# Optimization experiments

Measured on AMD Instinct MI355X. Metric: run time of the kernel, lower is better.

## Reference

```python
import jax, jax.numpy as jnp
import numpy as np

N_NODES = 100000
N_EDGES = 3200000
N_GRAPHS = 512
DIM_H = 128
N_LAYERS = 3
N_CLASSES = 10
BN_EPS = 1e-5


def setup_inputs() -> dict:
    key = jax.random.key(0)
    ks = jax.random.split(key, 16)
    s = 1.0 / np.sqrt(DIM_H)
    x = jax.random.normal(ks[0], (N_NODES, DIM_H), dtype=jnp.float32)
    edge_index = jax.random.randint(ks[1], (2, N_EDGES), 0, N_NODES, dtype=jnp.int64)
    batch = jnp.sort(jax.random.randint(ks[2], (N_NODES,), 0, N_GRAPHS, dtype=jnp.int64))
    W1 = jax.random.uniform(ks[3], (N_LAYERS, DIM_H, DIM_H), jnp.float32, -s, s)
    b1 = jax.random.uniform(ks[4], (N_LAYERS, DIM_H), jnp.float32, -s, s)
    gamma = jnp.ones((N_LAYERS, DIM_H), jnp.float32)
    beta = jnp.zeros((N_LAYERS, DIM_H), jnp.float32)
    rmean = 0.1 * jax.random.normal(ks[5], (N_LAYERS, DIM_H), dtype=jnp.float32)
    rvar = jax.random.uniform(ks[6], (N_LAYERS, DIM_H), jnp.float32, 0.5, 1.5)
    W2 = jax.random.uniform(ks[7], (N_LAYERS, DIM_H, DIM_H), jnp.float32, -s, s)
    b2 = jax.random.uniform(ks[8], (N_LAYERS, DIM_H), jnp.float32, -s, s)
    dcat = DIM_H * N_LAYERS
    sf = 1.0 / np.sqrt(dcat)
    Wfin = jax.random.uniform(ks[9], (dcat, dcat), jnp.float32, -sf, sf)
    bfin = jax.random.uniform(ks[10], (dcat,), jnp.float32, -sf, sf)
    Wout = jax.random.uniform(ks[11], (dcat, N_CLASSES), jnp.float32, -sf, sf)
    bout = jax.random.uniform(ks[12], (N_CLASSES,), jnp.float32, -sf, sf)
    return {"x": x, "edge_index": edge_index, "batch": batch, "num_layers": N_LAYERS,
            "W1": W1, "b1": b1, "gamma": gamma, "beta": beta, "rmean": rmean, "rvar": rvar,
            "W2": W2, "b2": b2, "Wfin": Wfin, "bfin": bfin, "Wout": Wout, "bout": bout}


def reference(x, edge_index, batch, num_layers, W1, b1, gamma, beta, rmean, rvar, W2, b2, Wfin, bfin, Wout, bout):
    src, dst = edge_index[0], edge_index[1]
    h = x
    pooled = []
    for i in range(num_layers):
        # GINConv (eps=0): MLP(x + sum_{j in N(i)} x_j)
        aggr = jax.ops.segment_sum(h[src], dst, num_segments=N_NODES)
        z = (h + aggr) @ W1[i] + b1[i]
        # BatchNorm1d in eval mode (running stats)
        z = gamma[i] * (z - rmean[i]) * jax.lax.rsqrt(rvar[i] + BN_EPS) + beta[i]
        z = jax.nn.relu(z)
        h = jax.nn.relu(z @ W2[i] + b2[i])
        # global_add_pool: segment-sum over graph ids
        pooled.append(jax.ops.segment_sum(h, batch, num_segments=N_GRAPHS))
    h_fin = jnp.concatenate(pooled, axis=1)  # [G, dim_h*num_layers]
    h_fin = jax.nn.relu(h_fin @ Wfin + bfin)
    # dropout p=0.5 is identity in eval mode
    logits = h_fin @ Wout + bout
    return logits, jax.nn.log_softmax(logits, axis=1)
```

## Files before the change

### kernel.cpp

```cpp
#include <hip/hip_runtime.h>
#include <stdint.h>

#define N_NODES 100000
#define N_EDGES 3200000
#define N_GRAPHS 512
#define DIM 128
#define M_PAD 100096
#define NGB (M_PAD / 256)
#define NBUCK 391
#define CAP 9216
#define TILE 4096
#define NTILE 782
#define XMM_NB 392

typedef __bf16 bf16x8 __attribute__((ext_vector_type(8)));
typedef float f32x4 __attribute__((ext_vector_type(4)));

__device__ __forceinline__ unsigned short f2bf(float f) {
  unsigned u = __float_as_uint(f);
  u = u + 0x7FFFu + ((u >> 16) & 1u);
  return (unsigned short)(u >> 16);
}
__device__ __forceinline__ float bflo(unsigned v) { return __uint_as_float(v << 16); }
__device__ __forceinline__ float bfhi(unsigned v) { return __uint_as_float(v & 0xFFFF0000u); }
__device__ __forceinline__ unsigned packbf(float a, float b) {
  return (unsigned)f2bf(a) | ((unsigned)f2bf(b) << 16);
}

__global__ void k_zero32(int* __restrict__ p, int n) {
  int i = blockIdx.x * 256 + threadIdx.x;
  if (i < n) p[i] = 0;
}

__global__ __launch_bounds__(256) void k_bucket(const int* __restrict__ ei,
                                                int* __restrict__ cnt,
                                                unsigned* __restrict__ rec) {
  __shared__ int hist[NBUCK];
  __shared__ int curs[NBUCK];
  int t = threadIdx.x;
  int base_e = blockIdx.x * TILE;
  int es[16], ed[16];
#pragma unroll
  for (int k = 0; k < 16; ++k) {
    int e = base_e + k * 256 + t;
    if (e < N_EDGES) { es[k] = ei[e]; ed[k] = ei[N_EDGES + e]; }
    else ed[k] = -1;
  }
  for (int i = t; i < NBUCK; i += 256) hist[i] = 0;
  __syncthreads();
#pragma unroll
  for (int k = 0; k < 16; ++k)
    if (ed[k] >= 0) atomicAdd(&hist[ed[k] >> 8], 1);
  __syncthreads();
  for (int i = t; i < NBUCK; i += 256) {
    int h = hist[i];
    int g = h ? atomicAdd(&cnt[i], h) : 0;
    curs[i] = i * CAP + g;
  }
  __syncthreads();
#pragma unroll
  for (int k = 0; k < 16; ++k) {
    if (ed[k] >= 0) {
      int b = ed[k] >> 8;
      int pos = atomicAdd(&curs[b], 1);
      rec[pos] = ((unsigned)es[k] << 8) | (unsigned)(ed[k] & 255);
    }
  }
}

__global__ __launch_bounds__(512) void k_bscan(const int* __restrict__ cnt,
                                               int* __restrict__ bbase,
                                               int* __restrict__ row_ptr) {
  __shared__ int sc[512];
  int t = threadIdx.x;
  int tot = (t < NBUCK) ? min(cnt[t], CAP) : 0;
  sc[t] = tot; __syncthreads();
  for (int off = 1; off < 512; off <<= 1) {
    int x = (t >= off) ? sc[t - off] : 0;
    __syncthreads();
    sc[t] += x;
    __syncthreads();
  }
  if (t < NBUCK) bbase[t] = sc[t] - tot;
  if (t == NBUCK - 1) {
    bbase[NBUCK] = sc[t];
    row_ptr[N_NODES] = sc[t];
  }
}

__global__ __launch_bounds__(256) void k_build(const unsigned* __restrict__ rec,
                                               const int* __restrict__ cnt,
                                               const int* __restrict__ bbase,
                                               int* __restrict__ row_ptr,
                                               int* __restrict__ col) {
  __shared__ int hist[256];
  __shared__ int sc[256];
  __shared__ int curs[256];
  int b = blockIdx.x, t = threadIdx.x;
  int n = min(cnt[b], CAP);
  const unsigned* p = rec + (size_t)b * CAP;
  hist[t] = 0; __syncthreads();
  for (int i = t; i < n; i += 256) atomicAdd(&hist[p[i] & 255u], 1);
  __syncthreads();
  int v = hist[t];
  sc[t] = v; __syncthreads();
  for (int off = 1; off < 256; off <<= 1) {
    int x = (t >= off) ? sc[t - off] : 0;
    __syncthreads();
    sc[t] += x;
    __syncthreads();
  }
  int excl = bbase[b] + sc[t] - v;
  int node = (b << 8) + t;
  if (node < N_NODES) row_ptr[node] = excl;
  curs[t] = excl;
  __syncthreads();
  for (int i = t; i < n; i += 256) {
    unsigned w = p[i];
    int pos = atomicAdd(&curs[w & 255u], 1);
    col[pos] = (int)(w >> 8);
  }
}

__global__ void k_gptr(const int* __restrict__ batch, int* __restrict__ gptr) {
  int g = blockIdx.x * 64 + threadIdx.x;
  if (g > N_GRAPHS) return;
  int lo = 0, hi = N_NODES;
  while (lo < hi) { int mid = (lo + hi) >> 1; if (batch[mid] < g) lo = mid + 1; else hi = mid; }
  gptr[g] = lo;
}

__global__ __launch_bounds__(256) void k_xmm1(const float* __restrict__ x,
                                              float* __restrict__ pmax,
                                              float* __restrict__ pmin) {
  __shared__ float smx[8][32][4];
  __shared__ float smn[8][32][4];
  int t = threadIdx.x;
  int c4 = t & 31;
  int ro = t >> 5;
  float mx0 = 0.f, mx1 = 0.f, mx2 = 0.f, mx3 = 0.f;
  float mn0 = 0.f, mn1 = 0.f, mn2 = 0.f, mn3 = 0.f;
  for (int row = blockIdx.x * 8 + ro; row < N_NODES; row += XMM_NB * 8) {
    float4 v = ((const float4*)x)[(size_t)row * 32 + c4];
    mx0 = fmaxf(mx0, v.x); mn0 = fmaxf(mn0, -v.x);
    mx1 = fmaxf(mx1, v.y); mn1 = fmaxf(mn1, -v.y);
    mx2 = fmaxf(mx2, v.z); mn2 = fmaxf(mn2, -v.z);
    mx3 = fmaxf(mx3, v.w); mn3 = fmaxf(mn3, -v.w);
  }
  smx[ro][c4][0] = mx0; smx[ro][c4][1] = mx1; smx[ro][c4][2] = mx2; smx[ro][c4][3] = mx3;
  smn[ro][c4][0] = mn0; smn[ro][c4][1] = mn1; smn[ro][c4][2] = mn2; smn[ro][c4][3] = mn3;
  __syncthreads();
  for (int off = 4; off > 0; off >>= 1) {
    if (ro < off) {
#pragma unroll
      for (int k = 0; k < 4; ++k) {
        smx[ro][c4][k] = fmaxf(smx[ro][c4][k], smx[ro + off][c4][k]);
        smn[ro][c4][k] = fmaxf(smn[ro][c4][k], smn[ro + off][c4][k]);
      }
    }
    __syncthreads();
  }
  if (ro == 0) {
#pragma unroll
    for (int k = 0; k < 4; ++k) {
      pmax[blockIdx.x * 128 + c4 * 4 + k] = smx[0][c4][k];
      pmin[blockIdx.x * 128 + c4 * 4 + k] = smn[0][c4][k];
    }
  }
}

__global__ __launch_bounds__(64) void k_xmm2(const float* __restrict__ pmax,
                                             const float* __restrict__ pmin,
                                             float* __restrict__ xmx,
                                             float* __restrict__ xminf) {
  int c = blockIdx.x & 127;
  int isMin = blockIdx.x >> 7;
  const float* src = isMin ? pmin : pmax;
  int l = threadIdx.x;
  float m = 0.f;
  for (int p2 = l; p2 < XMM_NB; p2 += 64) m = fmaxf(m, src[p2 * 128 + c]);
#pragma unroll
  for (int off = 32; off > 0; off >>= 1) m = fmaxf(m, __shfl_down(m, off));
  if (l == 0) {
    if (isMin) xminf[c] = -m;
    else xmx[c] = m;
  }
}

__global__ __launch_bounds__(64) void k_hred(const float* __restrict__ pmaxb,
                                             float* __restrict__ hmax) {
  int c = blockIdx.x;
  float m = 0.f;
  for (int b = threadIdx.x; b < NGB; b += 64) m = fmaxf(m, pmaxb[(size_t)b * 128 + c]);
#pragma unroll
  for (int off = 32; off > 0; off >>= 1) m = fmaxf(m, __shfl_down(m, off));
  if (threadIdx.x == 0) hmax[c] = m;
}

__global__ void k_convx(const float* __restrict__ x, const float* __restrict__ qmin,
                        const float* __restrict__ qmax, unsigned short* __restrict__ xq) {
  int i = blockIdx.x * 256 + threadIdx.x;
  if (i >= M_PAD * 64) return;
  int lane = i & 63;
  unsigned short o = 0;
  if ((i >> 6) < N_NODES) {
    float mn0 = qmin[2 * lane], mn1 = qmin[2 * lane + 1];
    float r0 = qmax[2 * lane] - mn0, r1 = qmax[2 * lane + 1] - mn1;
    float is0 = r0 > 1e-20f ? 255.f / r0 : 0.f;
    float is1 = r1 > 1e-20f ? 255.f / r1 : 0.f;
    float2 f = ((const float2*)x)[i];
    int q0 = (int)rintf((f.x - mn0) * is0); q0 = min(max(q0, 0), 255);
    int q1 = (int)rintf((f.y - mn1) * is1); q1 = min(max(q1, 0), 255);
    o = (unsigned short)(q0 | (q1 << 8));
  }
  xq[i] = o;
}

__global__ void k_quant(const unsigned* __restrict__ hbf, const float* __restrict__ qmax,
                        unsigned short* __restrict__ hq) {
  int i = blockIdx.x * 256 + threadIdx.x;
  if (i >= M_PAD * 64) return;
  int lane = i & 63;
  float mx0 = qmax[2 * lane], mx1 = qmax[2 * lane + 1];
  float is0 = mx0 > 1e-20f ? 255.f / mx0 : 0.f;
  float is1 = mx1 > 1e-20f ? 255.f / mx1 : 0.f;
  unsigned v = hbf[i];
  int q0 = (int)rintf(bflo(v) * is0); q0 = min(max(q0, 0), 255);
  int q1 = (int)rintf(bfhi(v) * is1); q1 = min(max(q1, 0), 255);
  hq[i] = (unsigned short)(q0 | (q1 << 8));
}

__global__ void k_convw(const float* __restrict__ W1, const float* __restrict__ W2,
                        unsigned short* __restrict__ Wt1, unsigned short* __restrict__ Wt2) {
  int i = blockIdx.x * 256 + threadIdx.x;
  if (i >= 3 * DIM * DIM) return;
  int l = i >> 14, rem = i & 16383, k = rem >> 7, n = rem & 127;
  int o = (l << 14) + (n << 7) + k;
  Wt1[o] = f2bf(W1[i]);
  Wt2[o] = f2bf(W2[i]);
}

__global__ void k_coef(const float* __restrict__ b1, const float* __restrict__ gamma,
                       const float* __restrict__ beta, const float* __restrict__ rmean,
                       const float* __restrict__ rvar, const float* __restrict__ b2,
                       float* __restrict__ sA1, float* __restrict__ sB1,
                       float* __restrict__ sA2, float* __restrict__ sB2) {
  int i = blockIdx.x * 128 + threadIdx.x;
  if (i >= 3 * DIM) return;
  float sa = gamma[i] * rsqrtf(rvar[i] + 1e-5f);
  sA1[i] = sa;
  sB1[i] = fmaf(sa, b1[i] - rmean[i], beta[i]);
  sA2[i] = 1.0f;
  sB2[i] = b2[i];
}

__global__ __launch_bounds__(256) void k_aggr(const unsigned short* __restrict__ hq,
                                              const int* __restrict__ row_ptr,
                                              const int* __restrict__ col,
                                              const float* __restrict__ qmin,
                                              const float* __restrict__ qmax,
                                              unsigned* __restrict__ tmp) {
  int wv = (blockIdx.x << 2) + (threadIdx.x >> 6);
  int lane = threadIdx.x & 63;
  if (wv >= M_PAD) return;
  if (wv >= N_NODES) { tmp[wv * 64 + lane] = 0u; return; }
  float mn0 = qmin[2 * lane], mn1 = qmin[2 * lane + 1];
  float sc0 = (qmax[2 * lane] - mn0) * (1.0f / 255.0f);
  float sc1 = (qmax[2 * lane + 1] - mn1) * (1.0f / 255.0f);
  unsigned sv = hq[(size_t)wv * 64 + lane];
  int ia0 = (int)(sv & 255u), ia1 = (int)(sv >> 8);
  int s = __builtin_amdgcn_readfirstlane(row_ptr[wv]);
  int e = __builtin_amdgcn_readfirstlane(row_ptr[wv + 1]);
  for (int base = s; base < e; base += 64) {
    int n = e - base; if (n > 64) n = 64;
    int cv = (lane < n) ? col[base + lane] : 0;
    int j = 0;
    for (; j + 8 <= n; j += 8) {
      int c0 = __builtin_amdgcn_readlane(cv, j + 0);
      int c1 = __builtin_amdgcn_readlane(cv, j + 1);
      int c2 = __builtin_amdgcn_readlane(cv, j + 2);
      int c3 = __builtin_amdgcn_readlane(cv, j + 3);
      int c4 = __builtin_amdgcn_readlane(cv, j + 4);
      int c5 = __builtin_amdgcn_readlane(cv, j + 5);
      int c6 = __builtin_amdgcn_readlane(cv, j + 6);
      int c7 = __builtin_amdgcn_readlane(cv, j + 7);
      unsigned v0 = hq[(size_t)c0 * 64 + lane];
      unsigned v1 = hq[(size_t)c1 * 64 + lane];
      unsigned v2 = hq[(size_t)c2 * 64 + lane];
      unsigned v3 = hq[(size_t)c3 * 64 + lane];
      unsigned v4 = hq[(size_t)c4 * 64 + lane];
      unsigned v5 = hq[(size_t)c5 * 64 + lane];
      unsigned v6 = hq[(size_t)c6 * 64 + lane];
      unsigned v7 = hq[(size_t)c7 * 64 + lane];
      ia0 += (int)(v0 & 255u) + (int)(v1 & 255u) + (int)(v2 & 255u) + (int)(v3 & 255u)
           + (int)(v4 & 255u) + (int)(v5 & 255u) + (int)(v6 & 255u) + (int)(v7 & 255u);
      ia1 += (int)(v0 >> 8) + (int)(v1 >> 8) + (int)(v2 >> 8) + (int)(v3 >> 8)
           + (int)(v4 >> 8) + (int)(v5 >> 8) + (int)(v6 >> 8) + (int)(v7 >> 8);
    }
    for (; j < n; ++j) {
      int c = __builtin_amdgcn_readlane(cv, j);
      unsigned v = hq[(size_t)c * 64 + lane];
      ia0 += (int)(v & 255u); ia1 += (int)(v >> 8);
    }
  }
  float cnt = (float)(e - s + 1);
  float A0 = fmaf(mn0, cnt, sc0 * (float)ia0);
  float A1 = fmaf(mn1, cnt, sc1 * (float)ia1);
  tmp[wv * 64 + lane] = packbf(A0, A1);
}

__global__ __launch_bounds__(256, 2) void k_gemm(const unsigned short* __restrict__ A,
                                                 const unsigned short* __restrict__ Wt,
                                                 const float* __restrict__ sA,
                                                 const float* __restrict__ sB,
                                                 unsigned short* __restrict__ out,
                                                 float* __restrict__ pmaxb, int do_max) {
  __shared__ float colred[128];
  int w = threadIdx.x >> 6, lane = threadIdx.x & 63;
  int q = lane >> 4, n16 = lane & 15;
  int rbase = (blockIdx.x << 8) + (w << 6);
  if (do_max && threadIdx.x < 128) colred[threadIdx.x] = 0.f;

  bf16x8 Bf[4][8];
#pragma unroll
  for (int ks = 0; ks < 4; ++ks)
#pragma unroll
    for (int c = 0; c < 8; ++c)
      Bf[ks][c] = *(const bf16x8*)(Wt + (size_t)((c << 4) + n16) * DIM + ks * 32 + q * 8);

  float sc = sA[(0 << 4) + n16];
  (void)sc;
  float mcol[8];
#pragma unroll
  for (int c = 0; c < 8; ++c) mcol[c] = 0.f;

#pragma unroll
  for (int t = 0; t < 4; ++t) {
    int r0 = rbase + (t << 4);
    f32x4 acc[8] = {};
#pragma unroll
    for (int ks = 0; ks < 4; ++ks) {
      bf16x8 a = *(const bf16x8*)(A + (size_t)(r0 + n16) * DIM + ks * 32 + q * 8);
#pragma unroll
      for (int c = 0; c < 8; ++c)
        acc[c] = __builtin_amdgcn_mfma_f32_16x16x32_bf16(a, Bf[ks][c], acc[c], 0, 0, 0);
    }
#pragma unroll
    for (int c = 0; c < 8; ++c) {
      int colc = (c << 4) + n16;
      float s = sA[colc], tt = sB[colc];
#pragma unroll
      for (int r = 0; r < 4; ++r) {
        float v = fmaxf(fmaf(s, acc[c][r], tt), 0.0f);
        mcol[c] = fmaxf(mcol[c], v);
        out[(size_t)(r0 + (q << 2) + r) * DIM + colc] = f2bf(v);
      }
    }
  }

  if (do_max) {
    __syncthreads();
#pragma unroll
    for (int c = 0; c < 8; ++c)
      atomicMax((int*)&colred[(c << 4) + n16], __float_as_int(mcol[c]));
    __syncthreads();
    if (threadIdx.x < 128)
      pmaxb[(size_t)blockIdx.x * 128 + threadIdx.x] = colred[threadIdx.x];
  }
}

__global__ __launch_bounds__(256) void k_pool(const unsigned* __restrict__ hbf,
                                              const int* __restrict__ gptr,
                                              float* __restrict__ pooled, int layer) {
  __shared__ float red[4][128];
  int g = blockIdx.x;
  int uc = threadIdx.x & 63, rs = threadIdx.x >> 6;
  int beg = gptr[g], end = gptr[g + 1];
  float a0 = 0.f, a1 = 0.f;
  for (int r = beg + rs; r < end; r += 4) {
    unsigned v = hbf[(size_t)r * 64 + uc];
    a0 += bflo(v); a1 += bfhi(v);
  }
  red[rs][2 * uc] = a0; red[rs][2 * uc + 1] = a1;
  __syncthreads();
  if (rs == 0) {
    int c0 = 2 * uc, c1 = 2 * uc + 1;
    pooled[(size_t)g * 384 + layer * DIM + c0] = red[0][c0] + red[1][c0] + red[2][c0] + red[3][c0];
    pooled[(size_t)g * 384 + layer * DIM + c1] = red[0][c1] + red[1][c1] + red[2][c1] + red[3][c1];
  }
}

__global__ __launch_bounds__(384) void k_head(const float* __restrict__ pooled,
                                              const float* __restrict__ Wfin,
                                              const float* __restrict__ bfin,
                                              const float* __restrict__ Wout,
                                              const float* __restrict__ bout,
                                              float* __restrict__ out) {
  __shared__ float p[8][384];
  __shared__ float hf[8][392];
  __shared__ float lg[8][10];
  __shared__ float lse[8];
  int t = threadIdx.x, g0 = blockIdx.x << 3;
  for (int i = t; i < 8 * 384; i += 384)
    p[i / 384][i % 384] = pooled[(size_t)(g0 + i / 384) * 384 + (i % 384)];
  __syncthreads();
  float bb = bfin[t];
  float acc[8];
#pragma unroll
  for (int g = 0; g < 8; ++g) acc[g] = bb;
  for (int k = 0; k < 384; ++k) {
    float wv = Wfin[k * 384 + t];
#pragma unroll
    for (int g = 0; g < 8; ++g) acc[g] = fmaf(p[g][k], wv, acc[g]);
  }
#pragma unroll
  for (int g = 0; g < 8; ++g) hf[g][t] = fmaxf(acc[g], 0.f);
  __syncthreads();
  if (t < 80) {
    int g = t / 10, c = t % 10;
    float a = bout[c];
    for (int k = 0; k < 384; ++k) a = fmaf(hf[g][k], Wout[k * 10 + c], a);
    lg[g][c] = a;
  }
  __syncthreads();
  if (t < 8) {
    float m = lg[t][0];
#pragma unroll
    for (int i = 1; i < 10; ++i) m = fmaxf(m, lg[t][i]);
    float ss = 0.f;
#pragma unroll
    for (int i = 0; i < 10; ++i) ss += __expf(lg[t][i] - m);
    lse[t] = m + __logf(ss);
  }
  __syncthreads();
  if (t < 80) {
    int g = t / 10, c = t % 10;
    out[(size_t)(g0 + g) * 10 + c] = lg[g][c];
    out[(size_t)N_GRAPHS * 10 + (size_t)(g0 + g) * 10 + c] = lg[g][c] - lse[g];
  }
}

extern "C" void kernel_launch(void* const* d_in, const int* in_sizes, int n_in,
                              void* d_out, int out_size, void* d_ws, size_t ws_size,
                              hipStream_t stream) {
  const float* x     = (const float*)d_in[0];
  const int*   ei    = (const int*)d_in[1];
  const int*   batch = (const int*)d_in[2];
  const float* W1    = (const float*)d_in[4];
  const float* b1    = (const float*)d_in[5];
  const float* gamma = (const float*)d_in[6];
  const float* beta  = (const float*)d_in[7];
  const float* rmean = (const float*)d_in[8];
  const float* rvar  = (const float*)d_in[9];
  const float* W2    = (const float*)d_in[10];
  const float* b2    = (const float*)d_in[11];
  const float* Wfin  = (const float*)d_in[12];
  const float* bfin  = (const float*)d_in[13];
  const float* Wout  = (const float*)d_in[14];
  const float* bout  = (const float*)d_in[15];
  float* out = (float*)d_out;

  char* p = (char*)d_ws;
  auto alloc = [&](size_t bytes) { char* r = p; p += (bytes + 255) & ~255ull; return r; };
  int* cnt      = (int*)alloc(NBUCK * 4);
  unsigned* rec = (unsigned*)alloc((size_t)NBUCK * CAP * 4);
  int* bbase    = (int*)alloc((NBUCK + 1) * 4);
  int* row_ptr  = (int*)alloc((N_NODES + 1) * 4);
  int* colb     = (int*)alloc((size_t)N_EDGES * 4);
  int* gptr     = (int*)alloc((N_GRAPHS + 1) * 4);
  unsigned short* xq  = (unsigned short*)alloc((size_t)M_PAD * 64 * 2);
  unsigned short* hqb = (unsigned short*)alloc((size_t)M_PAD * 64 * 2);
  unsigned* hbf  = (unsigned*)alloc((size_t)M_PAD * 64 * 4);
  unsigned* tmpb = (unsigned*)alloc((size_t)M_PAD * 64 * 4);
  unsigned* zbuf = (unsigned*)alloc((size_t)M_PAD * 64 * 4);
  unsigned short* Wt1 = (unsigned short*)alloc(3 * DIM * DIM * 2);
  unsigned short* Wt2 = (unsigned short*)alloc(3 * DIM * DIM * 2);
  float* pmax   = (float*)alloc((size_t)XMM_NB * 128 * 4);
  float* pmin   = (float*)alloc((size_t)XMM_NB * 128 * 4);
  float* pmaxb  = (float*)alloc((size_t)NGB * 128 * 4);
  float* sA1    = (float*)alloc(384 * 4);
  float* sB1    = (float*)alloc(384 * 4);
  float* sA2    = (float*)alloc(384 * 4);
  float* sB2    = (float*)alloc(384 * 4);
  float* qbuf   = (float*)alloc(1024 * 4);
  float* xmx    = qbuf + 128;
  float* xminf  = qbuf + 256;
  float* hmax0  = qbuf + 384;
  float* hmax1  = qbuf + 512;
  float* zeros  = qbuf + 640;
  float* pooled = (float*)alloc((size_t)N_GRAPHS * 384 * 4);

  k_zero32<<<(NBUCK + 255) / 256, 256, 0, stream>>>(cnt, NBUCK);
  k_zero32<<<4, 256, 0, stream>>>((int*)qbuf, 1024);

  k_bucket<<<NTILE, 256, 0, stream>>>(ei, cnt, rec);
  k_bscan<<<1, 512, 0, stream>>>(cnt, bbase, row_ptr);
  k_build<<<NBUCK, 256, 0, stream>>>(rec, cnt, bbase, row_ptr, colb);
  k_gptr<<<9, 64, 0, stream>>>(batch, gptr);

  k_xmm1<<<XMM_NB, 256, 0, stream>>>(x, pmax, pmin);
  k_xmm2<<<256, 64, 0, stream>>>(pmax, pmin, xmx, xminf);
  k_convx<<<(M_PAD * 64 + 255) / 256, 256, 0, stream>>>(x, xminf, xmx, xq);
  k_convw<<<(3 * DIM * DIM + 255) / 256, 256, 0, stream>>>(W1, W2, Wt1, Wt2);
  k_coef<<<3, 128, 0, stream>>>(b1, gamma, beta, rmean, rvar, b2, sA1, sB1, sA2, sB2);

  k_aggr<<<M_PAD / 4, 256, 0, stream>>>(xq, row_ptr, colb, xminf, xmx, tmpb);
  k_gemm<<<NGB, 256, 0, stream>>>((const unsigned short*)tmpb, Wt1, sA1, sB1,
                                  (unsigned short*)zbuf, pmaxb, 0);
  k_gemm<<<NGB, 256, 0, stream>>>((const unsigned short*)zbuf, Wt2, sA2, sB2,
                                  (unsigned short*)hbf, pmaxb, 1);
  k_hred<<<128, 64, 0, stream>>>(pmaxb, hmax0);
  k_pool<<<N_GRAPHS, 256, 0, stream>>>(hbf, gptr, pooled, 0);
  k_quant<<<(M_PAD * 64 + 255) / 256, 256, 0, stream>>>(hbf, hmax0, hqb);
  k_aggr<<<M_PAD / 4, 256, 0, stream>>>(hqb, row_ptr, colb, zeros, hmax0, tmpb);
  k_gemm<<<NGB, 256, 0, stream>>>((const unsigned short*)tmpb, Wt1 + DIM * DIM,
                                  sA1 + DIM, sB1 + DIM, (unsigned short*)zbuf, pmaxb, 0);
  k_gemm<<<NGB, 256, 0, stream>>>((const unsigned short*)zbuf, Wt2 + DIM * DIM,
                                  sA2 + DIM, sB2 + DIM, (unsigned short*)hbf, pmaxb, 1);
  k_hred<<<128, 64, 0, stream>>>(pmaxb, hmax1);
  k_pool<<<N_GRAPHS, 256, 0, stream>>>(hbf, gptr, pooled, 1);
  k_quant<<<(M_PAD * 64 + 255) / 256, 256, 0, stream>>>(hbf, hmax1, hqb);
  k_aggr<<<M_PAD / 4, 256, 0, stream>>>(hqb, row_ptr, colb, zeros, hmax1, tmpb);
  k_gemm<<<NGB, 256, 0, stream>>>((const unsigned short*)tmpb, Wt1 + 2 * DIM * DIM,
                                  sA1 + 2 * DIM, sB1 + 2 * DIM, (unsigned short*)zbuf, pmaxb, 0);
  k_gemm<<<NGB, 256, 0, stream>>>((const unsigned short*)zbuf, Wt2 + 2 * DIM * DIM,
                                  sA2 + 2 * DIM, sB2 + 2 * DIM, (unsigned short*)hbf, pmaxb, 0);
  k_pool<<<N_GRAPHS, 256, 0, stream>>>(hbf, gptr, pooled, 2);

  k_head<<<N_GRAPHS / 8, 384, 0, stream>>>(pooled, Wfin, bfin, Wout, bout, out);
}
```

Measured before the change: 683.0 us.

## Fuse both MLP GEMMs via LDS and pair-edge packed SWAR gather in aggregation

The two per-layer GEMMs are merged into one kernel that keeps the intermediate activation tile in LDS, so the z buffer no longer makes a round trip through global memory and one launch per layer goes away. The aggregation kernel is rewritten so each wave processes two edges per load step: the two half-waves read 32-bit words holding four 8-bit values each, accumulate them with packed 16-bit SWAR adds, and combine the halves with a shuffle. This halves the number of gather load instructions. The costs are about 70KB of LDS per block, which may lower occupancy, and the packed 16-bit accumulators, which could overflow on very high-degree nodes.

```diff
diff --git a/kernel.cpp b/kernel.cpp
--- a/kernel.cpp
+++ b/kernel.cpp
@@ -260,112 +260,166 @@
                                               const float* __restrict__ qmin,
                                               const float* __restrict__ qmax,
                                               unsigned* __restrict__ tmp) {
+  const unsigned* hq32 = (const unsigned*)hq;
   int wv = (blockIdx.x << 2) + (threadIdx.x >> 6);
   int lane = threadIdx.x & 63;
+  int dw = lane & 31;
+  bool hi = lane >= 32;
   if (wv >= M_PAD) return;
-  if (wv >= N_NODES) { tmp[wv * 64 + lane] = 0u; return; }
-  float mn0 = qmin[2 * lane], mn1 = qmin[2 * lane + 1];
-  float sc0 = (qmax[2 * lane] - mn0) * (1.0f / 255.0f);
-  float sc1 = (qmax[2 * lane + 1] - mn1) * (1.0f / 255.0f);
-  unsigned sv = hq[(size_t)wv * 64 + lane];
-  int ia0 = (int)(sv & 255u), ia1 = (int)(sv >> 8);
+  if (wv >= N_NODES) {
+    ((uint2*)(tmp + (size_t)wv * 64))[dw] = make_uint2(0u, 0u);
+    return;
+  }
+  unsigned ae = 0u, ao = 0u;
   int s = __builtin_amdgcn_readfirstlane(row_ptr[wv]);
   int e = __builtin_amdgcn_readfirstlane(row_ptr[wv + 1]);
   for (int base = s; base < e; base += 64) {
     int n = e - base; if (n > 64) n = 64;
     int cv = (lane < n) ? col[base + lane] : 0;
+    int np = n >> 1;
     int j = 0;
-    for (; j + 8 <= n; j += 8) {
-      int c0 = __builtin_amdgcn_readlane(cv, j + 0);
-      int c1 = __builtin_amdgcn_readlane(cv, j + 1);
-      int c2 = __builtin_amdgcn_readlane(cv, j + 2);
-      int c3 = __builtin_amdgcn_readlane(cv, j + 3);
-      int c4 = __builtin_amdgcn_readlane(cv, j + 4);
-      int c5 = __builtin_amdgcn_readlane(cv, j + 5);
-      int c6 = __builtin_amdgcn_readlane(cv, j + 6);
-      int c7 = __builtin_amdgcn_readlane(cv, j + 7);
-      unsigned v0 = hq[(size_t)c0 * 64 + lane];
-      unsigned v1 = hq[(size_t)c1 * 64 + lane];
-      unsigned v2 = hq[(size_t)c2 * 64 + lane];
-      unsigned v3 = hq[(size_t)c3 * 64 + lane];
-      unsigned v4 = hq[(size_t)c4 * 64 + lane];
-      unsigned v5 = hq[(size_t)c5 * 64 + lane];
-      unsigned v6 = hq[(size_t)c6 * 64 + lane];
-      unsigned v7 = hq[(size_t)c7 * 64 + lane];
-      ia0 += (int)(v0 & 255u) + (int)(v1 & 255u) + (int)(v2 & 255u) + (int)(v3 & 255u)
-           + (int)(v4 & 255u) + (int)(v5 & 255u) + (int)(v6 & 255u) + (int)(v7 & 255u);
-      ia1 += (int)(v0 >> 8) + (int)(v1 >> 8) + (int)(v2 >> 8) + (int)(v3 >> 8)
-           + (int)(v4 >> 8) + (int)(v5 >> 8) + (int)(v6 >> 8) + (int)(v7 >> 8);
-    }
-    for (; j < n; ++j) {
-      int c = __builtin_amdgcn_readlane(cv, j);
-      unsigned v = hq[(size_t)c * 64 + lane];
-      ia0 += (int)(v & 255u); ia1 += (int)(v >> 8);
-    }
-  }
-  float cnt = (float)(e - s + 1);
-  float A0 = fmaf(mn0, cnt, sc0 * (float)ia0);
-  float A1 = fmaf(mn1, cnt, sc1 * (float)ia1);
-  tmp[wv * 64 + lane] = packbf(A0, A1);
-}
-
-__global__ __launch_bounds__(256, 2) void k_gemm(const unsigned short* __restrict__ A,
-                                                 const unsigned short* __restrict__ Wt,
-                                                 const float* __restrict__ sA,
-                                                 const float* __restrict__ sB,
-                                                 unsigned short* __restrict__ out,
-                                                 float* __restrict__ pmaxb, int do_max) {
+    for (; j + 4 <= np; j += 4) {
+#pragma unroll
+      for (int u = 0; u < 4; ++u) {
+        int s0 = __builtin_amdgcn_readlane(cv, 2 * (j + u));
+        int s1 = __builtin_amdgcn_readlane(cv, 2 * (j + u) + 1);
+        int a0 = s0 * 32 + dw;
+        int a1 = s1 * 32 + dw;
+        unsigned v = hq32[hi ? a1 : a0];
+        ae += v & 0x00FF00FFu;
+        ao += (v >> 8) & 0x00FF00FFu;
+      }
+    }
+    for (; j < np; ++j) {
+      int s0 = __builtin_amdgcn_readlane(cv, 2 * j);
+      int s1 = __builtin_amdgcn_readlane(cv, 2 * j + 1);
+      int a0 = s0 * 32 + dw;
+      int a1 = s1 * 32 + dw;
+      unsigned v = hq32[hi ? a1 : a0];
+      ae += v & 0x00FF00FFu;
+      ao += (v >> 8) & 0x00FF00FFu;
+    }
+    if (n & 1) {
+      int c = __builtin_amdgcn_readlane(cv, n - 1);
+      unsigned v = hq32[c * 32 + dw];
+      if (hi) v = 0u;
+      ae += v & 0x00FF00FFu;
+      ao += (v >> 8) & 0x00FF00FFu;
+    }
+  }
+  ae += __shfl_xor(ae, 32);
+  ao += __shfl_xor(ao, 32);
+  {
+    unsigned v = hq32[wv * 32 + dw];
+    ae += v & 0x00FF00FFu;
+    ao += (v >> 8) & 0x00FF00FFu;
+  }
+  if (lane < 32) {
+    float cnt = (float)(e - s + 1);
+    float4 qn = ((const float4*)qmin)[dw];
+    float4 qx = ((const float4*)qmax)[dw];
+    float s0f = (float)(ae & 0xFFFFu);
+    float s1f = (float)(ao & 0xFFFFu);
+    float s2f = (float)(ae >> 16);
+    float s3f = (float)(ao >> 16);
+    const float k255 = 1.0f / 255.0f;
+    float A0 = fmaf(qn.x, cnt, (qx.x - qn.x) * k255 * s0f);
+    float A1 = fmaf(qn.y, cnt, (qx.y - qn.y) * k255 * s1f);
+    float A2 = fmaf(qn.z, cnt, (qx.z - qn.z) * k255 * s2f);
+    float A3 = fmaf(qn.w, cnt, (qx.w - qn.w) * k255 * s3f);
+    ((uint2*)(tmp + (size_t)wv * 64))[dw] = make_uint2(packbf(A0, A1), packbf(A2, A3));
+  }
+}
+
+__global__ __launch_bounds__(256, 2) void k_gemm12(const unsigned short* __restrict__ A,
+                                                   const unsigned short* __restrict__ Wt1,
+                                                   const float* __restrict__ sA1,
+                                                   const float* __restrict__ sB1,
+                                                   const unsigned short* __restrict__ Wt2,
+                                                   const float* __restrict__ sA2,
+                                                   const float* __restrict__ sB2,
+                                                   unsigned short* __restrict__ out,
+                                                   float* __restrict__ pmaxb, int do_max) {
+  __shared__ unsigned short zt[4][64][136];
   __shared__ float colred[128];
   int w = threadIdx.x >> 6, lane = threadIdx.x & 63;
   int q = lane >> 4, n16 = lane & 15;
   int rbase = (blockIdx.x << 8) + (w << 6);
   if (do_max && threadIdx.x < 128) colred[threadIdx.x] = 0.f;
 
-  bf16x8 Bf[4][8];
-#pragma unroll
-  for (int ks = 0; ks < 4; ++ks)
-#pragma unroll
-    for (int c = 0; c < 8; ++c)
-      Bf[ks][c] = *(const bf16x8*)(Wt + (size_t)((c << 4) + n16) * DIM + ks * 32 + q * 8);
-
-  float sc = sA[(0 << 4) + n16];
-  (void)sc;
-  float mcol[8];
-#pragma unroll
-  for (int c = 0; c < 8; ++c) mcol[c] = 0.f;
-
-#pragma unroll
-  for (int t = 0; t < 4; ++t) {
-    int r0 = rbase + (t << 4);
-    f32x4 acc[8] = {};
-#pragma unroll
-    for (int ks = 0; ks < 4; ++ks) {
-      bf16x8 a = *(const bf16x8*)(A + (size_t)(r0 + n16) * DIM + ks * 32 + q * 8);
+  {
+    bf16x8 Bf[4][8];
+#pragma unroll
+    for (int ks = 0; ks < 4; ++ks)
 #pragma unroll
       for (int c = 0; c < 8; ++c)
-        acc[c] = __builtin_amdgcn_mfma_f32_16x16x32_bf16(a, Bf[ks][c], acc[c], 0, 0, 0);
-    }
-#pragma unroll
-    for (int c = 0; c < 8; ++c) {
-      int colc = (c << 4) + n16;
-      float s = sA[colc], tt = sB[colc];
-#pragma unroll
-      for (int r = 0; r < 4; ++r) {
-        float v = fmaxf(fmaf(s, acc[c][r], tt), 0.0f);
-        mcol[c] = fmaxf(mcol[c], v);
-        out[(size_t)(r0 + (q << 2) + r) * DIM + colc] = f2bf(v);
+        Bf[ks][c] = *(const bf16x8*)(Wt1 + (size_t)((c << 4) + n16) * DIM + ks * 32 + q * 8);
+#pragma unroll
+    for (int t = 0; t < 4; ++t) {
+      int r0 = rbase + (t << 4);
+      f32x4 acc[8] = {};
+#pragma unroll
+      for (int ks = 0; ks < 4; ++ks) {
+        bf16x8 a = *(const bf16x8*)(A + (size_t)(r0 + n16) * DIM + ks * 32 + q * 8);
+#pragma unroll
+        for (int c = 0; c < 8; ++c)
+          acc[c] = __builtin_amdgcn_mfma_f32_16x16x32_bf16(a, Bf[ks][c], acc[c], 0, 0, 0);
       }
-    }
-  }
-
-  if (do_max) {
-    __syncthreads();
-#pragma unroll
-    for (int c = 0; c < 8; ++c)
-      atomicMax((int*)&colred[(c << 4) + n16], __float_as_int(mcol[c]));
-    __syncthreads();
-    if (threadIdx.x < 128)
-      pmaxb[(size_t)blockIdx.x * 128 + threadIdx.x] = colred[threadIdx.x];
+#pragma unroll
+      for (int c = 0; c < 8; ++c) {
+        int colc = (c << 4) + n16;
+        float s = sA1[colc], tt = sB1[colc];
+#pragma unroll
+        for (int r = 0; r < 4; ++r) {
+          float v = fmaxf(fmaf(s, acc[c][r], tt), 0.0f);
+          zt[w][(t << 4) + (q << 2) + r][colc] = f2bf(v);
+        }
+      }
+    }
+  }
+
+  {
+    bf16x8 Bf[4][8];
+#pragma unroll
+    for (int ks = 0; ks < 4; ++ks)
+#pragma unroll
+      for (int c = 0; c < 8; ++c)
+        Bf[ks][c] = *(const bf16x8*)(Wt2 + (size_t)((c << 4) + n16) * DIM + ks * 32 + q * 8);
+    float mcol[8];
+#pragma unroll
+    for (int c = 0; c < 8; ++c) mcol[c] = 0.f;
+#pragma unroll
+    for (int t = 0; t < 4; ++t) {
+      int r0 = rbase + (t << 4);
+      f32x4 acc[8] = {};
+#pragma unroll
+      for (int ks = 0; ks < 4; ++ks) {
+        bf16x8 a = *(const bf16x8*)(&zt[w][(t << 4) + n16][ks * 32 + q * 8]);
+#pragma unroll
+        for (int c = 0; c < 8; ++c)
+          acc[c] = __builtin_amdgcn_mfma_f32_16x16x32_bf16(a, Bf[ks][c], acc[c], 0, 0, 0);
+      }
+#pragma unroll
+      for (int c = 0; c < 8; ++c) {
+        int colc = (c << 4) + n16;
+        float s = sA2[colc], tt = sB2[colc];
+#pragma unroll
+        for (int r = 0; r < 4; ++r) {
+          float v = fmaxf(fmaf(s, acc[c][r], tt), 0.0f);
+          mcol[c] = fmaxf(mcol[c], v);
+          out[(size_t)(r0 + (q << 2) + r) * DIM + colc] = f2bf(v);
+        }
+      }
+    }
+    if (do_max) {
+      __syncthreads();
+#pragma unroll
+      for (int c = 0; c < 8; ++c)
+        atomicMax((int*)&colred[(c << 4) + n16], __float_as_int(mcol[c]));
+      __syncthreads();
+      if (threadIdx.x < 128)
+        pmaxb[(size_t)blockIdx.x * 128 + threadIdx.x] = colred[threadIdx.x];
+    }
   }
 }
 
@@ -472,7 +526,6 @@
   unsigned short* hqb = (unsigned short*)alloc((size_t)M_PAD * 64 * 2);
   unsigned* hbf  = (unsigned*)alloc((size_t)M_PAD * 64 * 4);
   unsigned* tmpb = (unsigned*)alloc((size_t)M_PAD * 64 * 4);
-  unsigned* zbuf = (unsigned*)alloc((size_t)M_PAD * 64 * 4);
   unsigned short* Wt1 = (unsigned short*)alloc(3 * DIM * DIM * 2);
   unsigned short* Wt2 = (unsigned short*)alloc(3 * DIM * DIM * 2);
   float* pmax   = (float*)alloc((size_t)XMM_NB * 128 * 4);
@@ -505,26 +558,22 @@
   k_coef<<<3, 128, 0, stream>>>(b1, gamma, beta, rmean, rvar, b2, sA1, sB1, sA2, sB2);
 
   k_aggr<<<M_PAD / 4, 256, 0, stream>>>(xq, row_ptr, colb, xminf, xmx, tmpb);
-  k_gemm<<<NGB, 256, 0, stream>>>((const unsigned short*)tmpb, Wt1, sA1, sB1,
-                                  (unsigned short*)zbuf, pmaxb, 0);
-  k_gemm<<<NGB, 256, 0, stream>>>((const unsigned short*)zbuf, Wt2, sA2, sB2,
-                                  (unsigned short*)hbf, pmaxb, 1);
+  k_gemm12<<<NGB, 256, 0, stream>>>((const unsigned short*)tmpb, Wt1, sA1, sB1,
+                                    Wt2, sA2, sB2, (unsigned short*)hbf, pmaxb, 1);
   k_hred<<<128, 64, 0, stream>>>(pmaxb, hmax0);
   k_pool<<<N_GRAPHS, 256, 0, stream>>>(hbf, gptr, pooled, 0);
   k_quant<<<(M_PAD * 64 + 255) / 256, 256, 0, stream>>>(hbf, hmax0, hqb);
   k_aggr<<<M_PAD / 4, 256, 0, stream>>>(hqb, row_ptr, colb, zeros, hmax0, tmpb);
-  k_gemm<<<NGB, 256, 0, stream>>>((const unsigned short*)tmpb, Wt1 + DIM * DIM,
-                                  sA1 + DIM, sB1 + DIM, (unsigned short*)zbuf, pmaxb, 0);
-  k_gemm<<<NGB, 256, 0, stream>>>((const unsigned short*)zbuf, Wt2 + DIM * DIM,
-                                  sA2 + DIM, sB2 + DIM, (unsigned short*)hbf, pmaxb, 1);
+  k_gemm12<<<NGB, 256, 0, stream>>>((const unsigned short*)tmpb, Wt1 + DIM * DIM,
+                                    sA1 + DIM, sB1 + DIM, Wt2 + DIM * DIM,
+                                    sA2 + DIM, sB2 + DIM, (unsigned short*)hbf, pmaxb, 1);
   k_hred<<<128, 64, 0, stream>>>(pmaxb, hmax1);
   k_pool<<<N_GRAPHS, 256, 0, stream>>>(hbf, gptr, pooled, 1);
   k_quant<<<(M_PAD * 64 + 255) / 256, 256, 0, stream>>>(hbf, hmax1, hqb);
   k_aggr<<<M_PAD / 4, 256, 0, stream>>>(hqb, row_ptr, colb, zeros, hmax1, tmpb);
-  k_gemm<<<NGB, 256, 0, stream>>>((const unsigned short*)tmpb, Wt1 + 2 * DIM * DIM,
-                                  sA1 + 2 * DIM, sB1 + 2 * DIM, (unsigned short*)zbuf, pmaxb, 0);
-  k_gemm<<<NGB, 256, 0, stream>>>((const unsigned short*)zbuf, Wt2 + 2 * DIM * DIM,
-                                  sA2 + 2 * DIM, sB2 + 2 * DIM, (unsigned short*)hbf, pmaxb, 0);
+  k_gemm12<<<NGB, 256, 0, stream>>>((const unsigned short*)tmpb, Wt1 + 2 * DIM * DIM,
+                                    sA1 + 2 * DIM, sB1 + 2 * DIM, Wt2 + 2 * DIM * DIM,
+                                    sA2 + 2 * DIM, sB2 + 2 * DIM, (unsigned short*)hbf, pmaxb, 0);
   k_pool<<<N_GRAPHS, 256, 0, stream>>>(hbf, gptr, pooled, 2);
 
   k_head<<<N_GRAPHS / 8, 384, 0, stream>>>(pooled, Wfin, bfin, Wout, bout, out);
```

Result: faster. 662.8 us (-3.0%).
